# Kernel optimization log

Hardware: AMD Instinct MI355X
Metric: run time of the kernel (lower is better)

## Reference

```python
import jax, jax.numpy as jnp
import numpy as np

# Lorentz (hyperboloid) manifold, curvature parameter K: x0 = sqrt(K + ||x_space||^2)
K = 1.0
LN_EPS = 1e-5
PROJ_EPS = 1e-6
L, D, H, B, S, V = 12, 512, 8, 2, 1024, 50257
DH = D // H  # 64 space dims per head


def add_time(space):
    # lift space components onto the hyperboloid
    t = jnp.sqrt(jnp.sum(space * space, axis=-1, keepdims=True) + K)
    return jnp.concatenate([t, space], axis=-1)


def l_project(z):
    # renormalize an ambient vector onto the hyperboloid (Lorentz midpoint / LResNet normalization)
    inner = -jnp.square(z[..., :1]) + jnp.sum(jnp.square(z[..., 1:]), axis=-1, keepdims=True)
    return jnp.sqrt(K) * z / jnp.sqrt(jnp.clip(-inner, PROJ_EPS, None))


def l_layernorm(x, g, b):
    # LayerNorm on the space part, recompute time
    s = x[..., 1:]
    mu = jnp.mean(s, axis=-1, keepdims=True)
    var = jnp.var(s, axis=-1, keepdims=True)
    s = (s - mu) * jax.lax.rsqrt(var + LN_EPS) * g + b
    return add_time(s)


def setup_inputs() -> dict:
    key = jax.random.key(0)
    ks = jax.random.split(key, 12)
    std_in = D ** -0.5
    std_out = (2 * D * L) ** -0.5  # out_proj_std from the torch init
    inp = {}
    inp['text_tokens'] = jax.random.randint(ks[0], (B, S), 0, V)
    inp['embed_table'] = jax.random.normal(ks[1], (V, D - 1), jnp.float32) * 0.02
    inp['Wq'] = jax.random.normal(ks[2], (L, D, D), jnp.float32) * std_in
    inp['bq'] = jnp.zeros((L, D), jnp.float32)
    inp['Wk'] = jax.random.normal(ks[3], (L, D, D), jnp.float32) * std_in
    inp['bk'] = jnp.zeros((L, D), jnp.float32)
    inp['Wv'] = jax.random.normal(ks[4], (L, D, D), jnp.float32) * std_in
    inp['bv'] = jnp.zeros((L, D), jnp.float32)
    inp['Wo'] = jax.random.normal(ks[5], (L, H * (DH + 1), D - 1), jnp.float32) * std_in
    inp['bo'] = jnp.zeros((L, D - 1), jnp.float32)
    inp['ln1_g'] = jnp.ones((L, D - 1), jnp.float32)
    inp['ln1_b'] = jnp.zeros((L, D - 1), jnp.float32)
    inp['ln2_g'] = jnp.ones((L, D - 1), jnp.float32)
    inp['ln2_b'] = jnp.zeros((L, D - 1), jnp.float32)
    inp['Wfc'] = jax.random.normal(ks[6], (L, D, 4 * D - 1), jnp.float32) * std_in
    inp['bfc'] = jnp.zeros((L, 4 * D - 1), jnp.float32)
    inp['Wpr'] = jax.random.normal(ks[7], (L, 4 * D, D - 1), jnp.float32) * std_out
    inp['bpr'] = jnp.zeros((L, D - 1), jnp.float32)
    inp['res_w1'] = jnp.ones((L,), jnp.float32)
    inp['res_w2'] = jnp.ones((L,), jnp.float32)
    inp['Wfin'] = jax.random.normal(ks[8], (D, D - 1), jnp.float32) * std_in
    inp['bfin'] = jnp.zeros((D - 1,), jnp.float32)
    inp['lnf_g'] = jnp.ones((D - 1,), jnp.float32)
    inp['lnf_b'] = jnp.zeros((D - 1,), jnp.float32)
    return inp


def reference(text_tokens, embed_table, Wq, bq, Wk, bk, Wv, bv, Wo, bo, ln1_g, ln1_b,
              ln2_g, ln2_b, Wfc, bfc, Wpr, bpr, res_w1, res_w2, Wfin, bfin, lnf_g, lnf_b):
    b, s = text_tokens.shape
    scale = 1.0 / np.sqrt(DH)
    # LorentzEmbeddings: space-part lookup, time recomputed
    x = add_time(embed_table[text_tokens])  # [B, S, D]
    causal = jnp.tril(jnp.ones((s, s), bool))  # True = attend
    for i in range(L):
        # --- Lorentz multi-head self-attention ---
        lx = l_layernorm(x, ln1_g[i], ln1_b[i])
        q = add_time((lx @ Wq[i] + bq[i]).reshape(b, s, H, DH))  # [B,S,H,DH+1]
        k = add_time((lx @ Wk[i] + bk[i]).reshape(b, s, H, DH))
        v = add_time((lx @ Wv[i] + bv[i]).reshape(b, s, H, DH))
        qm = jnp.concatenate([-q[..., :1], q[..., 1:]], axis=-1)  # apply Minkowski metric
        linner = jnp.einsum('bihd,bjhd->bhij', qm, k)  # Lorentz inner product <q_i, k_j>_L
        scores = (2.0 * K + 2.0 * linner) * scale     # = -d_L^2(q,k)/sqrt(dh)
        scores = jnp.where(causal[None, None], scores, -1e9)
        a = jax.nn.softmax(scores, axis=-1)
        agg = jnp.einsum('bhij,bjhd->bihd', a, v)      # Lorentz centroid numerator
        agg = l_project(agg)                           # normalize back to hyperboloid
        ax = add_time(agg.reshape(b, s, H * (DH + 1)) @ Wo[i] + bo[i])  # heads-concat proj
        x = l_project(x + res_w1[i] * ax)              # LResNet residual 1
        # --- Lorentz MLP ---
        h = l_layernorm(x, ln2_g[i], ln2_b[i])
        h = add_time(h @ Wfc[i] + bfc[i])              # c_fc: D -> 4D ambient
        h = add_time(jax.nn.gelu(h[..., 1:]))          # LorentzActivation (GELU on space)
        h = add_time(h @ Wpr[i] + bpr[i])              # c_proj: 4D -> D ambient
        x = l_project(x + res_w2[i] * h)               # LResNet residual 2
    x = add_time(x @ Wfin + bfin)                      # final_proj
    x = l_layernorm(x, lnf_g, lnf_b)                   # ln_final
    return x
```

## Files before the change

kernel.cpp:

```cpp
#include <hip/hip_runtime.h>
#include <cstdint>

#define DEV __device__ __forceinline__

typedef _Float16 f16;
typedef _Float16 f16x8 __attribute__((ext_vector_type(8)));
typedef float f32x4 __attribute__((ext_vector_type(4)));
typedef unsigned int u32;

DEV void gll16(const void* g, void* l) {
  __builtin_amdgcn_global_load_lds((const __attribute__((address_space(1))) u32*)g,
                                   (__attribute__((address_space(3))) u32*)l, 16, 0, 0);
}

DEV float block_sum(float v, float* red) {
#pragma unroll
  for (int o = 32; o; o >>= 1) v += __shfl_xor(v, o);
  int w = threadIdx.x >> 6;
  __syncthreads();
  if ((threadIdx.x & 63) == 0) red[w] = v;
  __syncthreads();
  return red[0] + red[1] + red[2] + red[3];
}

__global__ void k_trans(const float* __restrict__ W, f16* __restrict__ BT, int K, int N, int Kpad) {
  __shared__ float t[32][33];
  int n0 = blockIdx.x * 32, k0 = blockIdx.y * 32, tx = threadIdx.x, ty = threadIdx.y;
  for (int i = ty; i < 32; i += 8) {
    int k = k0 + i, n = n0 + tx;
    t[i][tx] = (k < K && n < N) ? W[(size_t)k * N + n] : 0.f;
  }
  __syncthreads();
  for (int i = ty; i < 32; i += 8)
    BT[(size_t)(n0 + i) * Kpad + k0 + tx] = (f16)t[tx][i];
}

__global__ void k_trans3(const float* __restrict__ Wq, const float* __restrict__ Wk,
                         const float* __restrict__ Wv, f16* __restrict__ BT) {
  __shared__ float t[32][33];
  const float* W = (blockIdx.z == 0) ? Wq : (blockIdx.z == 1) ? Wk : Wv;
  f16* dst = BT + (size_t)blockIdx.z * 512 * 512;
  int n0 = blockIdx.x * 32, k0 = blockIdx.y * 32, tx = threadIdx.x, ty = threadIdx.y;
  for (int i = ty; i < 32; i += 8) t[i][tx] = W[(size_t)(k0 + i) * 512 + n0 + tx];
  __syncthreads();
  for (int i = ty; i < 32; i += 8) dst[(size_t)(n0 + i) * 512 + k0 + tx] = (f16)t[tx][i];
}

template <int BM, int BN>
__launch_bounds__(256)
__global__ void k_gemm(const f16* __restrict__ A, const f16* __restrict__ BT,
                       float* __restrict__ C, int K, int Nstride) {
  constexpr int BK = 32;
  constexpr int FM = BM / 32, FN = BN / 32;
  __shared__ f16 sA[BM * BK];
  __shared__ f16 sB[BN * BK];
  const int tid = threadIdx.x, wid = tid >> 6, lane = tid & 63;
  const int m0 = blockIdx.x * BM, n0 = blockIdx.y * BN;
  const int wm = wid >> 1, wn = wid & 1;
  f32x4 acc[FM][FN];
#pragma unroll
  for (int i = 0; i < FM; i++)
#pragma unroll
    for (int j = 0; j < FN; j++) acc[i][j] = (f32x4){0.f, 0.f, 0.f, 0.f};
  const char* Ab = (const char*)A + (size_t)m0 * K * 2;
  const char* Bb = (const char*)BT + (size_t)n0 * K * 2;
  const size_t rowB = (size_t)K * 2;
  for (int k0 = 0; k0 < K; k0 += BK) {
    for (int i = wid; i < BM / 16; i += 4)
      gll16(Ab + (size_t)(i * 16 + (lane >> 2)) * rowB + k0 * 2 + (lane & 3) * 16,
            (char*)sA + i * 1024);
    for (int i = wid; i < BN / 16; i += 4)
      gll16(Bb + (size_t)(i * 16 + (lane >> 2)) * rowB + k0 * 2 + (lane & 3) * 16,
            (char*)sB + i * 1024);
    __syncthreads();
    f16x8 af[FM], bfr[FN];
#pragma unroll
    for (int i = 0; i < FM; i++)
      af[i] = *(const f16x8*)(sA + (wm * (BM / 2) + i * 16 + (lane & 15)) * BK + (lane >> 4) * 8);
#pragma unroll
    for (int j = 0; j < FN; j++)
      bfr[j] = *(const f16x8*)(sB + (wn * (BN / 2) + j * 16 + (lane & 15)) * BK + (lane >> 4) * 8);
#pragma unroll
    for (int i = 0; i < FM; i++)
#pragma unroll
      for (int j = 0; j < FN; j++)
        acc[i][j] = __builtin_amdgcn_mfma_f32_16x16x32_f16(af[i], bfr[j], acc[i][j], 0, 0, 0);
    __syncthreads();
  }
#pragma unroll
  for (int i = 0; i < FM; i++) {
    int row0 = m0 + wm * (BM / 2) + i * 16 + ((lane >> 4) * 4);
#pragma unroll
    for (int j = 0; j < FN; j++) {
      int col = n0 + wn * (BN / 2) + j * 16 + (lane & 15);
#pragma unroll
      for (int r = 0; r < 4; r++) C[(size_t)(row0 + r) * Nstride + col] = acc[i][j][r];
    }
  }
}

__global__ void k_embed(const int* __restrict__ tok, const float* __restrict__ tbl,
                        const float* __restrict__ g, const float* __restrict__ bsh,
                        float* __restrict__ x, f16* __restrict__ act) {
  __shared__ float red[4];
  const int m = blockIdx.x, tid = threadIdx.x;
  const float* e = tbl + (size_t)tok[m] * 511;
  float e0 = (tid < 511) ? e[tid] : 0.f;
  float e1 = (tid + 256 < 511) ? e[tid + 256] : 0.f;
  float s1 = block_sum(e0 + e1, red);
  float s2 = block_sum(e0 * e0 + e1 * e1, red);
  float t = sqrtf(s2 + 1.f);
  float* xr = x + (size_t)m * 512;
  if (tid == 0) xr[0] = t;
  if (tid < 511) xr[1 + tid] = e0;
  if (tid + 256 < 511) xr[257 + tid] = e1;
  float mu = s1 / 511.f;
  float var = s2 / 511.f - mu * mu;
  float inv = rsqrtf(var + 1e-5f);
  float n0 = (tid < 511) ? (e0 - mu) * inv * g[tid] + bsh[tid] : 0.f;
  float n1 = (tid + 256 < 511) ? (e1 - mu) * inv * g[tid + 256] + bsh[tid + 256] : 0.f;
  float sn = block_sum(n0 * n0 + n1 * n1, red);
  float t2 = sqrtf(sn + 1.f);
  f16* ar = act + (size_t)m * 512;
  if (tid == 0) ar[0] = (f16)t2;
  if (tid < 511) ar[1 + tid] = (f16)n0;
  if (tid + 256 < 511) ar[257 + tid] = (f16)n1;
}

__launch_bounds__(64)
__global__ void k_qkvsplit(const float* __restrict__ raw, const float* __restrict__ bq,
                           const float* __restrict__ bk, const float* __restrict__ bv,
                           f16* __restrict__ qhat, f16* __restrict__ khat, f16* __restrict__ vT) {
  const int m = blockIdx.x, grp = blockIdx.y, typ = grp >> 3, h = grp & 7, lane = threadIdx.x;
  const float* bb = (typ == 0) ? bq : (typ == 1) ? bk : bv;
  float v = raw[(size_t)m * 1536 + typ * 512 + h * 64 + lane] + bb[h * 64 + lane];
  float s2 = v * v;
#pragma unroll
  for (int o = 32; o; o >>= 1) s2 += __shfl_xor(s2, o);
  float t = sqrtf(s2 + 1.0f);
  const int b = m >> 10, s = m & 1023, bh = b * 8 + h;
  if (typ == 0) {
    size_t base = ((size_t)bh * 1024 + s) * 88;
    qhat[base + lane] = (f16)(0.25f * v);
    if (lane == 0) qhat[base + 64] = (f16)(0.25f * t);
  } else if (typ == 1) {
    size_t base = ((size_t)bh * 1024 + s) * 88;
    khat[base + lane] = (f16)v;
    if (lane == 0) khat[base + 64] = (f16)t;
  } else {
    vT[((size_t)bh * 80 + lane) * 1024 + s] = (f16)v;
    if (lane == 0) vT[((size_t)bh * 80 + 64) * 1024 + s] = (f16)t;
  }
}

__launch_bounds__(256)
__global__ void k_attn(const f16* __restrict__ qhat, const f16* __restrict__ khat,
                       const f16* __restrict__ vT, f16* __restrict__ ao) {
  __shared__ f16 sK[64 * 88];
  __shared__ f16 sV[80 * 72];
  __shared__ f16 sP[4][16 * 80];
  const int bh = blockIdx.x, qt = blockIdx.y, q0 = qt * 64;
  const int tid = threadIdx.x, wid = tid >> 6, lane = tid & 63;
  const int l15 = lane & 15, l4 = lane >> 4;
  const f16* qpl = qhat + (size_t)bh * 1024 * 88;
  const f16* kpl = khat + (size_t)bh * 1024 * 88;
  const f16* vpl = vT + (size_t)bh * 80 * 1024;
  const int qrow = q0 + wid * 16;
  f16x8 qf0 = *(const f16x8*)(qpl + (size_t)(qrow + l15) * 88 + l4 * 8);
  f16x8 qf1 = *(const f16x8*)(qpl + (size_t)(qrow + l15) * 88 + 32 + l4 * 8);
  float qth[4];
#pragma unroll
  for (int r = 0; r < 4; r++) qth[r] = (float)qpl[(size_t)(qrow + l4 * 4 + r) * 88 + 64];
  f32x4 acc[5];
#pragma unroll
  for (int i = 0; i < 5; i++) acc[i] = (f32x4){0, 0, 0, 0};
  float mrun[4] = {-3e38f, -3e38f, -3e38f, -3e38f}, lrun[4] = {0, 0, 0, 0};
  const int ntiles = qt + 1;
  for (int jt = 0; jt < ntiles; ++jt) {
    int j0 = jt * 64;
    for (int i = wid; i < 11; i += 4)
      gll16((const char*)kpl + (size_t)j0 * 176 + i * 1024 + lane * 16, (char*)sK + i * 1024);
    for (int idx = tid; idx < 640; idx += 256) {
      int row = idx >> 3, c = idx & 7;
      *(int4*)(sV + row * 72 + c * 8) = *(const int4*)(vpl + (size_t)row * 1024 + j0 + c * 8);
    }
    __syncthreads();
    f32x4 sc[4];
#pragma unroll
    for (int fn = 0; fn < 4; fn++) {
      const f16* kb = sK + (fn * 16 + l15) * 88;
      f16x8 k0v = *(const f16x8*)(kb + l4 * 8);
      f16x8 k1v = *(const f16x8*)(kb + 32 + l4 * 8);
      f32x4 a = (f32x4){0, 0, 0, 0};
      a = __builtin_amdgcn_mfma_f32_16x16x32_f16(qf0, k0v, a, 0, 0, 0);
      a = __builtin_amdgcn_mfma_f32_16x16x32_f16(qf1, k1v, a, 0, 0, 0);
      sc[fn] = a;
    }
    float s[4][4];
#pragma unroll
    for (int fn = 0; fn < 4; fn++) {
      float ktc = (float)sK[(fn * 16 + l15) * 88 + 64];
      int col = j0 + fn * 16 + l15;
#pragma unroll
      for (int r = 0; r < 4; r++) {
        int row = q0 + wid * 16 + l4 * 4 + r;
        float v = sc[fn][r] - qth[r] * ktc;
        s[fn][r] = (col <= row) ? v : -3e38f;
      }
    }
    float mnew[4], al[4], rs[4];
#pragma unroll
    for (int r = 0; r < 4; r++) {
      float t = fmaxf(fmaxf(s[0][r], s[1][r]), fmaxf(s[2][r], s[3][r]));
#pragma unroll
      for (int o = 8; o; o >>= 1) t = fmaxf(t, __shfl_xor(t, o));
      mnew[r] = fmaxf(mrun[r], t);
      al[r] = exp2f((mrun[r] - mnew[r]) * 1.44269504f);
      mrun[r] = mnew[r];
      rs[r] = 0.f;
    }
    f16* sPw = sP[wid];
#pragma unroll
    for (int fn = 0; fn < 4; fn++)
#pragma unroll
      for (int r = 0; r < 4; r++) {
        float p = exp2f((s[fn][r] - mnew[r]) * 1.44269504f);
        rs[r] += p;
        sPw[(l4 * 4 + r) * 80 + fn * 16 + l15] = (f16)p;
      }
#pragma unroll
    for (int r = 0; r < 4; r++) {
#pragma unroll
      for (int o = 8; o; o >>= 1) rs[r] += __shfl_xor(rs[r], o);
      lrun[r] = lrun[r] * al[r] + rs[r];
    }
#pragma unroll
    for (int fd = 0; fd < 5; fd++)
#pragma unroll
      for (int r = 0; r < 4; r++) acc[fd][r] *= al[r];
#pragma unroll
    for (int ks = 0; ks < 2; ks++) {
      f16x8 pf = *(const f16x8*)(sPw + l15 * 80 + ks * 32 + l4 * 8);
#pragma unroll
      for (int fd = 0; fd < 5; fd++) {
        f16x8 vf = *(const f16x8*)(sV + (fd * 16 + l15) * 72 + ks * 32 + l4 * 8);
        acc[fd] = __builtin_amdgcn_mfma_f32_16x16x32_f16(pf, vf, acc[fd], 0, 0, 0);
      }
    }
    __syncthreads();
  }
  const int b = bh >> 3, h = bh & 7;
#pragma unroll
  for (int r = 0; r < 4; r++) {
    float invl = 1.0f / lrun[r];
    float ss = 0.f;
    float ov[4];
#pragma unroll
    for (int fd = 0; fd < 4; fd++) {
      ov[fd] = acc[fd][r] * invl;
      ss += ov[fd] * ov[fd];
    }
#pragma unroll
    for (int o = 8; o; o >>= 1) ss += __shfl_xor(ss, o);
    float tv = acc[4][r] * invl;
    tv = __shfl(tv, lane & 48);
    float scp = rsqrtf(fmaxf(tv * tv - ss, 1e-6f));
    int row = q0 + wid * 16 + l4 * 4 + r;
    size_t rb = ((size_t)b * 1024 + row) * 544 + h * 65;
    if (l15 == 0) ao[rb] = (f16)(tv * scp);
#pragma unroll
    for (int fd = 0; fd < 4; fd++) ao[rb + 1 + fd * 16 + l15] = (f16)(ov[fd] * scp);
  }
}

__global__ void k_resproj(float* __restrict__ x, const float* __restrict__ raw,
                          const float* __restrict__ bias, const float* __restrict__ resw, int li,
                          const float* __restrict__ g, const float* __restrict__ bsh,
                          f16* __restrict__ act, int applyLN) {
  __shared__ float red[4];
  const int m = blockIdx.x, tid = threadIdx.x;
  const float* rr = raw + (size_t)m * 512;
  float* xr = x + (size_t)m * 512;
  const float rw = resw[li];
  float y0 = (tid < 511) ? rr[tid] + bias[tid] : 0.f;
  float y1 = (tid + 256 < 511) ? rr[tid + 256] + bias[tid + 256] : 0.f;
  float s2 = block_sum(y0 * y0 + y1 * y1, red);
  float tax = sqrtf(s2 + 1.f);
  float xt = xr[0];
  float u0 = (tid < 511) ? xr[1 + tid] + rw * y0 : 0.f;
  float u1 = (tid + 256 < 511) ? xr[257 + tid] + rw * y1 : 0.f;
  float ut = xt + rw * tax;
  float su = block_sum(u0 + u1, red);
  float su2 = block_sum(u0 * u0 + u1 * u1, red);
  float scp = rsqrtf(fmaxf(ut * ut - su2, 1e-6f));
  float nx0 = u0 * scp, nx1 = u1 * scp, nxt = ut * scp;
  if (tid == 0) xr[0] = nxt;
  if (tid < 511) xr[1 + tid] = nx0;
  if (tid + 256 < 511) xr[257 + tid] = nx1;
  f16* ar = act + (size_t)m * 512;
  if (applyLN) {
    float mu = su * scp / 511.f;
    float var = su2 * scp * scp / 511.f - mu * mu;
    float inv = rsqrtf(var + 1e-5f);
    float n0 = (tid < 511) ? (nx0 - mu) * inv * g[tid] + bsh[tid] : 0.f;
    float n1 = (tid + 256 < 511) ? (nx1 - mu) * inv * g[tid + 256] + bsh[tid + 256] : 0.f;
    float sn = block_sum(n0 * n0 + n1 * n1, red);
    float t2 = sqrtf(sn + 1.f);
    if (tid == 0) ar[0] = (f16)t2;
    if (tid < 511) ar[1 + tid] = (f16)n0;
    if (tid + 256 < 511) ar[257 + tid] = (f16)n1;
  } else {
    if (tid == 0) ar[0] = (f16)nxt;
    if (tid < 511) ar[1 + tid] = (f16)nx0;
    if (tid + 256 < 511) ar[257 + tid] = (f16)nx1;
  }
}

__global__ void k_gelu(const float* __restrict__ raw, const float* __restrict__ bias,
                       f16* __restrict__ act) {
  __shared__ float red[4];
  const int m = blockIdx.x, tid = threadIdx.x;
  const float* rr = raw + (size_t)m * 2048;
  float gv[8];
  float s2 = 0.f;
#pragma unroll
  for (int i = 0; i < 8; i++) {
    int j = i * 256 + tid;
    float y = (j < 2047) ? rr[j] + bias[j] : 0.f;
    float c = y * y * y;
    float gg = 0.5f * y * (1.f + tanhf(0.7978845608f * (y + 0.044715f * c)));
    if (j >= 2047) gg = 0.f;
    gv[i] = gg;
    s2 += gg * gg;
  }
  s2 = block_sum(s2, red);
  float t = sqrtf(s2 + 1.f);
  f16* ar = act + (size_t)m * 2048;
  if (tid == 0) ar[0] = (f16)t;
#pragma unroll
  for (int i = 0; i < 8; i++) {
    int j = i * 256 + tid;
    if (j < 2047) ar[1 + j] = (f16)gv[i];
  }
}

__global__ void k_final(const float* __restrict__ raw, const float* __restrict__ bias,
                        const float* __restrict__ g, const float* __restrict__ bsh,
                        float* __restrict__ out) {
  __shared__ float red[4];
  const int m = blockIdx.x, tid = threadIdx.x;
  const float* rr = raw + (size_t)m * 512;
  float y0 = (tid < 511) ? rr[tid] + bias[tid] : 0.f;
  float y1 = (tid + 256 < 511) ? rr[tid + 256] + bias[tid + 256] : 0.f;
  float s1 = block_sum(y0 + y1, red);
  float s2 = block_sum(y0 * y0 + y1 * y1, red);
  float mu = s1 / 511.f;
  float var = s2 / 511.f - mu * mu;
  float inv = rsqrtf(var + 1e-5f);
  float n0 = (tid < 511) ? (y0 - mu) * inv * g[tid] + bsh[tid] : 0.f;
  float n1 = (tid + 256 < 511) ? (y1 - mu) * inv * g[tid + 256] + bsh[tid + 256] : 0.f;
  float sn = block_sum(n0 * n0 + n1 * n1, red);
  float t2 = sqrtf(sn + 1.f);
  float* orow = out + (size_t)m * 512;
  if (tid == 0) orow[0] = t2;
  if (tid < 511) orow[1 + tid] = n0;
  if (tid + 256 < 511) orow[257 + tid] = n1;
}

extern "C" void kernel_launch(void* const* d_in, const int* in_sizes, int n_in,
                              void* d_out, int out_size, void* d_ws, size_t ws_size,
                              hipStream_t stream) {
  (void)in_sizes; (void)n_in; (void)out_size; (void)ws_size;
  const int* tok = (const int*)d_in[0];
  const float* etab = (const float*)d_in[1];
  const float* Wq = (const float*)d_in[2];
  const float* bq = (const float*)d_in[3];
  const float* Wk = (const float*)d_in[4];
  const float* bk = (const float*)d_in[5];
  const float* Wv = (const float*)d_in[6];
  const float* bv = (const float*)d_in[7];
  const float* Wo = (const float*)d_in[8];
  const float* bo = (const float*)d_in[9];
  const float* ln1g = (const float*)d_in[10];
  const float* ln1b = (const float*)d_in[11];
  const float* ln2g = (const float*)d_in[12];
  const float* ln2b = (const float*)d_in[13];
  const float* Wfc = (const float*)d_in[14];
  const float* bfc = (const float*)d_in[15];
  const float* Wpr = (const float*)d_in[16];
  const float* bpr = (const float*)d_in[17];
  const float* rw1 = (const float*)d_in[18];
  const float* rw2 = (const float*)d_in[19];
  const float* Wfin = (const float*)d_in[20];
  const float* bfin = (const float*)d_in[21];
  const float* lnfg = (const float*)d_in[22];
  const float* lnfb = (const float*)d_in[23];

  char* wsb = (char*)d_ws;
  size_t off = 0;
  auto alloc = [&](size_t bytes) -> char* {
    char* p = wsb + off;
    off = (off + bytes + 1023) & ~(size_t)1023;
    return p;
  };
  float* x = (float*)alloc(2048ull * 512 * 4);
  f16* actA = (f16*)alloc(2048ull * 512 * 2);
  float* raw = (float*)alloc(2048ull * 2048 * 4);
  f16* qhat = (f16*)alloc(16ull * 1024 * 88 * 2);
  f16* khat = (f16*)alloc(16ull * 1024 * 88 * 2);
  f16* vT = (f16*)alloc(16ull * 80 * 1024 * 2);
  f16* ao = (f16*)alloc(2048ull * 544 * 2);
  f16* fcact = (f16*)alloc(2048ull * 2048 * 2);
  f16* wqkvT = (f16*)alloc(1536ull * 512 * 2);
  f16* woT = (f16*)alloc(512ull * 544 * 2);
  f16* wfcT = (f16*)alloc(2048ull * 512 * 2);
  f16* wprT = (f16*)alloc(512ull * 2048 * 2);
  f16* wfinT = (f16*)alloc(512ull * 512 * 2);

  k_embed<<<2048, 256, 0, stream>>>(tok, etab, ln1g, ln1b, x, actA);

  for (int li = 0; li < 12; li++) {
    const float* Wq_l = Wq + (size_t)li * 512 * 512;
    const float* Wk_l = Wk + (size_t)li * 512 * 512;
    const float* Wv_l = Wv + (size_t)li * 512 * 512;
    const float* Wo_l = Wo + (size_t)li * 520 * 511;
    const float* Wfc_l = Wfc + (size_t)li * 512 * 2047;
    const float* Wpr_l = Wpr + (size_t)li * 2048 * 511;
    const float* bq_l = bq + (size_t)li * 512;
    const float* bk_l = bk + (size_t)li * 512;
    const float* bv_l = bv + (size_t)li * 512;
    const float* bo_l = bo + (size_t)li * 511;
    const float* bfc_l = bfc + (size_t)li * 2047;
    const float* bpr_l = bpr + (size_t)li * 511;
    const float* ln2g_l = ln2g + (size_t)li * 511;
    const float* ln2b_l = ln2b + (size_t)li * 511;

    k_trans3<<<dim3(16, 16, 3), dim3(32, 8), 0, stream>>>(Wq_l, Wk_l, Wv_l, wqkvT);
    k_trans<<<dim3(16, 17), dim3(32, 8), 0, stream>>>(Wo_l, woT, 520, 511, 544);
    k_trans<<<dim3(64, 16), dim3(32, 8), 0, stream>>>(Wfc_l, wfcT, 512, 2047, 512);
    k_trans<<<dim3(16, 64), dim3(32, 8), 0, stream>>>(Wpr_l, wprT, 2048, 511, 2048);

    k_gemm<128, 128><<<dim3(16, 12), 256, 0, stream>>>(actA, wqkvT, raw, 512, 1536);
    k_qkvsplit<<<dim3(2048, 24), 64, 0, stream>>>(raw, bq_l, bk_l, bv_l, qhat, khat, vT);
    k_attn<<<dim3(16, 16), 256, 0, stream>>>(qhat, khat, vT, ao);
    k_gemm<64, 64><<<dim3(32, 8), 256, 0, stream>>>(ao, woT, raw, 544, 512);
    k_resproj<<<2048, 256, 0, stream>>>(x, raw, bo_l, rw1, li, ln2g_l, ln2b_l, actA, 1);
    k_gemm<128, 128><<<dim3(16, 16), 256, 0, stream>>>(actA, wfcT, raw, 512, 2048);
    k_gelu<<<2048, 256, 0, stream>>>(raw, bfc_l, fcact);
    k_gemm<64, 64><<<dim3(32, 8), 256, 0, stream>>>(fcact, wprT, raw, 2048, 512);
    const float* ng = (li < 11) ? ln1g + (size_t)(li + 1) * 511 : ln1g;
    const float* nb = (li < 11) ? ln1b + (size_t)(li + 1) * 511 : ln1b;
    k_resproj<<<2048, 256, 0, stream>>>(x, raw, bpr_l, rw2, li, ng, nb, actA, (li < 11) ? 1 : 0);
  }

  k_trans<<<dim3(16, 16), dim3(32, 8), 0, stream>>>(Wfin, wfinT, 512, 511, 512);
  k_gemm<64, 64><<<dim3(32, 8), 256, 0, stream>>>(actA, wfinT, raw, 512, 512);
  k_final<<<2048, 256, 0, stream>>>(raw, bfin, lnfg, lnfb, (float*)d_out);
}
```

Baseline: 1.953 ms.

## Fuse QKV split and GELU into GEMM epilogues, batch weight transposes, rework attention

```diff
diff --git a/kernel.cpp b/kernel.cpp
--- a/kernel.cpp
+++ b/kernel.cpp
@@ -23,8 +23,11 @@
   return red[0] + red[1] + red[2] + red[3];
 }
 
-__global__ void k_trans(const float* __restrict__ W, f16* __restrict__ BT, int K, int N, int Kpad) {
+__global__ void k_trans(const float* __restrict__ W0, f16* __restrict__ BT0, int K, int N, int Kpad,
+                        size_t srcStride, size_t dstStride) {
   __shared__ float t[32][33];
+  const float* W = W0 + (size_t)blockIdx.z * srcStride;
+  f16* BT = BT0 + (size_t)blockIdx.z * dstStride;
   int n0 = blockIdx.x * 32, k0 = blockIdx.y * 32, tx = threadIdx.x, ty = threadIdx.y;
   for (int i = ty; i < 32; i += 8) {
     int k = k0 + i, n = n0 + tx;
@@ -38,63 +41,157 @@
 __global__ void k_trans3(const float* __restrict__ Wq, const float* __restrict__ Wk,
                          const float* __restrict__ Wv, f16* __restrict__ BT) {
   __shared__ float t[32][33];
-  const float* W = (blockIdx.z == 0) ? Wq : (blockIdx.z == 1) ? Wk : Wv;
-  f16* dst = BT + (size_t)blockIdx.z * 512 * 512;
+  const int layer = blockIdx.z / 3, typ = blockIdx.z % 3;
+  const float* W = ((typ == 0) ? Wq : (typ == 1) ? Wk : Wv) + (size_t)layer * 262144;
+  f16* dst = BT + (size_t)layer * 786432 + (size_t)typ * 262144;
   int n0 = blockIdx.x * 32, k0 = blockIdx.y * 32, tx = threadIdx.x, ty = threadIdx.y;
   for (int i = ty; i < 32; i += 8) t[i][tx] = W[(size_t)(k0 + i) * 512 + n0 + tx];
   __syncthreads();
   for (int i = ty; i < 32; i += 8) dst[(size_t)(n0 + i) * 512 + k0 + tx] = (f16)t[tx][i];
 }
 
-template <int BM, int BN>
+template <int BM, int BN, int EPI>
 __launch_bounds__(256)
 __global__ void k_gemm(const f16* __restrict__ A, const f16* __restrict__ BT,
-                       float* __restrict__ C, int K, int Nstride) {
-  constexpr int BK = 32;
+                       int lda, int ldb, int klen,
+                       float* __restrict__ O1, float* __restrict__ O2, int ldc,
+                       const float* __restrict__ c0, const float* __restrict__ c1,
+                       const float* __restrict__ c2, float* __restrict__ ssq,
+                       f16* __restrict__ H1, f16* __restrict__ H2, f16* __restrict__ H3) {
   constexpr int FM = BM / 32, FN = BN / 32;
-  __shared__ f16 sA[BM * BK];
-  __shared__ f16 sB[BN * BK];
+  __shared__ f16 sA[BM * 64];
+  __shared__ f16 sB[BN * 64];
   const int tid = threadIdx.x, wid = tid >> 6, lane = tid & 63;
+  const int l15 = lane & 15, l4 = lane >> 4;
   const int m0 = blockIdx.x * BM, n0 = blockIdx.y * BN;
   const int wm = wid >> 1, wn = wid & 1;
+  const int kbeg = blockIdx.z * klen;
   f32x4 acc[FM][FN];
 #pragma unroll
   for (int i = 0; i < FM; i++)
 #pragma unroll
     for (int j = 0; j < FN; j++) acc[i][j] = (f32x4){0.f, 0.f, 0.f, 0.f};
-  const char* Ab = (const char*)A + (size_t)m0 * K * 2;
-  const char* Bb = (const char*)BT + (size_t)n0 * K * 2;
-  const size_t rowB = (size_t)K * 2;
-  for (int k0 = 0; k0 < K; k0 += BK) {
-    for (int i = wid; i < BM / 16; i += 4)
-      gll16(Ab + (size_t)(i * 16 + (lane >> 2)) * rowB + k0 * 2 + (lane & 3) * 16,
-            (char*)sA + i * 1024);
-    for (int i = wid; i < BN / 16; i += 4)
-      gll16(Bb + (size_t)(i * 16 + (lane >> 2)) * rowB + k0 * 2 + (lane & 3) * 16,
-            (char*)sB + i * 1024);
+  const size_t ldab = (size_t)lda * 2, ldbb = (size_t)ldb * 2;
+  const int swz = ((lane & 7) ^ (lane >> 3)) * 16;
+  const char* Ab = (const char*)A + (size_t)m0 * ldab + (size_t)(lane >> 3) * ldab + swz;
+  const char* Bb = (const char*)BT + (size_t)n0 * ldbb + (size_t)(lane >> 3) * ldbb + swz;
+  for (int k0 = kbeg; k0 < kbeg + klen; k0 += 64) {
+    for (int i = wid; i < BM / 8; i += 4)
+      gll16(Ab + (size_t)(i * 8) * ldab + (size_t)k0 * 2, (char*)sA + i * 1024);
+    for (int i = wid; i < BN / 8; i += 4)
+      gll16(Bb + (size_t)(i * 8) * ldbb + (size_t)k0 * 2, (char*)sB + i * 1024);
     __syncthreads();
-    f16x8 af[FM], bfr[FN];
-#pragma unroll
-    for (int i = 0; i < FM; i++)
-      af[i] = *(const f16x8*)(sA + (wm * (BM / 2) + i * 16 + (lane & 15)) * BK + (lane >> 4) * 8);
-#pragma unroll
-    for (int j = 0; j < FN; j++)
-      bfr[j] = *(const f16x8*)(sB + (wn * (BN / 2) + j * 16 + (lane & 15)) * BK + (lane >> 4) * 8);
-#pragma unroll
-    for (int i = 0; i < FM; i++)
-#pragma unroll
-      for (int j = 0; j < FN; j++)
-        acc[i][j] = __builtin_amdgcn_mfma_f32_16x16x32_f16(af[i], bfr[j], acc[i][j], 0, 0, 0);
+#pragma unroll
+    for (int kk = 0; kk < 2; kk++) {
+      f16x8 af[FM], bf[FN];
+#pragma unroll
+      for (int i = 0; i < FM; i++) {
+        int row = wm * (BM / 2) + i * 16 + l15;
+        af[i] = *(const f16x8*)(sA + row * 64 + (((kk * 4 + l4) ^ (l15 & 7)) * 8));
+      }
+#pragma unroll
+      for (int j = 0; j < FN; j++) {
+        int row = wn * (BN / 2) + j * 16 + l15;
+        bf[j] = *(const f16x8*)(sB + row * 64 + (((kk * 4 + l4) ^ (l15 & 7)) * 8));
+      }
+#pragma unroll
+      for (int i = 0; i < FM; i++)
+#pragma unroll
+        for (int j = 0; j < FN; j++)
+          acc[i][j] = __builtin_amdgcn_mfma_f32_16x16x32_f16(af[i], bf[j], acc[i][j], 0, 0, 0);
+    }
     __syncthreads();
   }
-#pragma unroll
-  for (int i = 0; i < FM; i++) {
-    int row0 = m0 + wm * (BM / 2) + i * 16 + ((lane >> 4) * 4);
-#pragma unroll
-    for (int j = 0; j < FN; j++) {
-      int col = n0 + wn * (BN / 2) + j * 16 + (lane & 15);
-#pragma unroll
-      for (int r = 0; r < 4; r++) C[(size_t)(row0 + r) * Nstride + col] = acc[i][j][r];
+  if (EPI == 0) {
+#pragma unroll
+    for (int i = 0; i < FM; i++) {
+      int row0 = m0 + wm * (BM / 2) + i * 16 + l4 * 4;
+#pragma unroll
+      for (int j = 0; j < FN; j++) {
+        int col = n0 + wn * (BN / 2) + j * 16 + l15;
+#pragma unroll
+        for (int r = 0; r < 4; r++) O1[(size_t)(row0 + r) * ldc + col] = acc[i][j][r];
+      }
+    }
+  } else if (EPI == 1) {
+    const int cb = (n0 >> 6) + wn;
+    const int typ = cb >> 3, h = cb & 7;
+    const float* bb = (typ == 0) ? c0 : (typ == 1) ? c1 : c2;
+    float bias_j[FN];
+#pragma unroll
+    for (int j = 0; j < FN; j++) bias_j[j] = bb[h * 64 + j * 16 + l15];
+    const float qs = (typ == 0) ? 0.25f : 1.0f;
+#pragma unroll
+    for (int i = 0; i < FM; i++) {
+#pragma unroll
+      for (int r = 0; r < 4; r++) {
+        float y[FN];
+        float ss = 0.f;
+#pragma unroll
+        for (int j = 0; j < FN; j++) {
+          y[j] = acc[i][j][r] + bias_j[j];
+          ss += y[j] * y[j];
+        }
+        ss += __shfl_xor(ss, 1); ss += __shfl_xor(ss, 2);
+        ss += __shfl_xor(ss, 4); ss += __shfl_xor(ss, 8);
+        float t = sqrtf(ss + 1.f);
+        int row = m0 + wm * 64 + i * 16 + l4 * 4 + r;
+        int b = row >> 10, s = row & 1023, bh = b * 8 + h;
+        if (typ < 2) {
+          f16* dst = (typ == 0) ? H1 : H2;
+          size_t base = ((size_t)bh * 1024 + s) * 88;
+#pragma unroll
+          for (int j = 0; j < FN; j++) dst[base + j * 16 + l15] = (f16)(qs * y[j]);
+          if (l15 == 0) dst[base + 64] = (f16)(qs * t);
+        } else {
+#pragma unroll
+          for (int j = 0; j < FN; j++)
+            H3[((size_t)bh * 80 + j * 16 + l15) * 1024 + s] = (f16)y[j];
+          if (l15 == 0) H3[((size_t)bh * 80 + 64) * 1024 + s] = (f16)t;
+        }
+      }
+    }
+  } else if (EPI == 2) {
+#pragma unroll
+    for (int i = 0; i < FM; i++) {
+#pragma unroll
+      for (int r = 0; r < 4; r++) {
+        int row = m0 + wm * 64 + i * 16 + l4 * 4 + r;
+        float ss = 0.f;
+#pragma unroll
+        for (int j = 0; j < FN; j++) {
+          int col = n0 + wn * 64 + j * 16 + l15;
+          float gg = 0.f;
+          if (col < 2047) {
+            float yv = acc[i][j][r] + c0[col];
+            float cc = yv * yv * yv;
+            gg = 0.5f * yv * (1.f + tanhf(0.7978845608f * (yv + 0.044715f * cc)));
+          }
+          ss += gg * gg;
+          H1[(size_t)row * 2048 + col] = (f16)gg;
+        }
+        ss += __shfl_xor(ss, 1); ss += __shfl_xor(ss, 2);
+        ss += __shfl_xor(ss, 4); ss += __shfl_xor(ss, 8);
+        if (l15 == 0) atomicAdd(ssq + row, ss);
+      }
+    }
+  } else {
+    float* O = blockIdx.z ? O2 : O1;
+#pragma unroll
+    for (int i = 0; i < FM; i++) {
+#pragma unroll
+      for (int r = 0; r < 4; r++) {
+        int row = m0 + wm * (BM / 2) + i * 16 + l4 * 4 + r;
+        float t = 0.f;
+        if (blockIdx.z == 0) t = sqrtf(ssq[row] + 1.f);
+#pragma unroll
+        for (int j = 0; j < FN; j++) {
+          int col = n0 + wn * (BN / 2) + j * 16 + l15;
+          float v = acc[i][j][r];
+          if (blockIdx.z == 0) v += t * ((col < 511) ? c0[col] : 0.f);
+          O[(size_t)row * ldc + col] = v;
+        }
+      }
     }
   }
 }
@@ -128,67 +225,31 @@
 }
 
 __launch_bounds__(64)
-__global__ void k_qkvsplit(const float* __restrict__ raw, const float* __restrict__ bq,
-                           const float* __restrict__ bk, const float* __restrict__ bv,
-                           f16* __restrict__ qhat, f16* __restrict__ khat, f16* __restrict__ vT) {
-  const int m = blockIdx.x, grp = blockIdx.y, typ = grp >> 3, h = grp & 7, lane = threadIdx.x;
-  const float* bb = (typ == 0) ? bq : (typ == 1) ? bk : bv;
-  float v = raw[(size_t)m * 1536 + typ * 512 + h * 64 + lane] + bb[h * 64 + lane];
-  float s2 = v * v;
-#pragma unroll
-  for (int o = 32; o; o >>= 1) s2 += __shfl_xor(s2, o);
-  float t = sqrtf(s2 + 1.0f);
-  const int b = m >> 10, s = m & 1023, bh = b * 8 + h;
-  if (typ == 0) {
-    size_t base = ((size_t)bh * 1024 + s) * 88;
-    qhat[base + lane] = (f16)(0.25f * v);
-    if (lane == 0) qhat[base + 64] = (f16)(0.25f * t);
-  } else if (typ == 1) {
-    size_t base = ((size_t)bh * 1024 + s) * 88;
-    khat[base + lane] = (f16)v;
-    if (lane == 0) khat[base + 64] = (f16)t;
-  } else {
-    vT[((size_t)bh * 80 + lane) * 1024 + s] = (f16)v;
-    if (lane == 0) vT[((size_t)bh * 80 + 64) * 1024 + s] = (f16)t;
-  }
-}
-
-__launch_bounds__(256)
 __global__ void k_attn(const f16* __restrict__ qhat, const f16* __restrict__ khat,
                        const f16* __restrict__ vT, f16* __restrict__ ao) {
-  __shared__ f16 sK[64 * 88];
-  __shared__ f16 sV[80 * 72];
-  __shared__ f16 sP[4][16 * 80];
-  const int bh = blockIdx.x, qt = blockIdx.y, q0 = qt * 64;
-  const int tid = threadIdx.x, wid = tid >> 6, lane = tid & 63;
-  const int l15 = lane & 15, l4 = lane >> 4;
-  const f16* qpl = qhat + (size_t)bh * 1024 * 88;
-  const f16* kpl = khat + (size_t)bh * 1024 * 88;
-  const f16* vpl = vT + (size_t)bh * 80 * 1024;
-  const int qrow = q0 + wid * 16;
-  f16x8 qf0 = *(const f16x8*)(qpl + (size_t)(qrow + l15) * 88 + l4 * 8);
-  f16x8 qf1 = *(const f16x8*)(qpl + (size_t)(qrow + l15) * 88 + 32 + l4 * 8);
+  __shared__ f16 sP[16 * 88];
+  const int bid = blockIdx.x, bh = bid & 15, rt = 63 - (bid >> 4);
+  const int lane = threadIdx.x, l15 = lane & 15, l4 = lane >> 4;
+  const f16* qp = qhat + ((size_t)bh * 1024 + rt * 16) * 88;
+  const f16* kp = khat + (size_t)bh * 1024 * 88;
+  const f16* vp = vT + (size_t)bh * 80 * 1024;
+  f16x8 qf0 = *(const f16x8*)(qp + l15 * 88 + l4 * 8);
+  f16x8 qf1 = *(const f16x8*)(qp + l15 * 88 + 32 + l4 * 8);
   float qth[4];
 #pragma unroll
-  for (int r = 0; r < 4; r++) qth[r] = (float)qpl[(size_t)(qrow + l4 * 4 + r) * 88 + 64];
+  for (int r = 0; r < 4; r++) qth[r] = (float)qp[(l4 * 4 + r) * 88 + 64];
   f32x4 acc[5];
 #pragma unroll
   for (int i = 0; i < 5; i++) acc[i] = (f32x4){0, 0, 0, 0};
   float mrun[4] = {-3e38f, -3e38f, -3e38f, -3e38f}, lrun[4] = {0, 0, 0, 0};
-  const int ntiles = qt + 1;
-  for (int jt = 0; jt < ntiles; ++jt) {
-    int j0 = jt * 64;
-    for (int i = wid; i < 11; i += 4)
-      gll16((const char*)kpl + (size_t)j0 * 176 + i * 1024 + lane * 16, (char*)sK + i * 1024);
-    for (int idx = tid; idx < 640; idx += 256) {
-      int row = idx >> 3, c = idx & 7;
-      *(int4*)(sV + row * 72 + c * 8) = *(const int4*)(vpl + (size_t)row * 1024 + j0 + c * 8);
-    }
-    __syncthreads();
+  const int nt = (rt >> 2) + 1;
+  for (int jt = 0; jt < nt; ++jt) {
+    const int j0 = jt * 64;
+    const bool dt = (jt == nt - 1);
     f32x4 sc[4];
 #pragma unroll
     for (int fn = 0; fn < 4; fn++) {
-      const f16* kb = sK + (fn * 16 + l15) * 88;
+      const f16* kb = kp + (size_t)(j0 + fn * 16 + l15) * 88;
       f16x8 k0v = *(const f16x8*)(kb + l4 * 8);
       f16x8 k1v = *(const f16x8*)(kb + 32 + l4 * 8);
       f32x4 a = (f32x4){0, 0, 0, 0};
@@ -199,13 +260,13 @@
     float s[4][4];
 #pragma unroll
     for (int fn = 0; fn < 4; fn++) {
-      float ktc = (float)sK[(fn * 16 + l15) * 88 + 64];
+      float ktc = (float)kp[(size_t)(j0 + fn * 16 + l15) * 88 + 64];
       int col = j0 + fn * 16 + l15;
 #pragma unroll
       for (int r = 0; r < 4; r++) {
-        int row = q0 + wid * 16 + l4 * 4 + r;
+        int row = rt * 16 + l4 * 4 + r;
         float v = sc[fn][r] - qth[r] * ktc;
-        s[fn][r] = (col <= row) ? v : -3e38f;
+        s[fn][r] = (!dt || col <= row) ? v : -3e38f;
       }
     }
     float mnew[4], al[4], rs[4];
@@ -219,14 +280,13 @@
       mrun[r] = mnew[r];
       rs[r] = 0.f;
     }
-    f16* sPw = sP[wid];
 #pragma unroll
     for (int fn = 0; fn < 4; fn++)
 #pragma unroll
       for (int r = 0; r < 4; r++) {
         float p = exp2f((s[fn][r] - mnew[r]) * 1.44269504f);
         rs[r] += p;
-        sPw[(l4 * 4 + r) * 80 + fn * 16 + l15] = (f16)p;
+        sP[(l4 * 4 + r) * 88 + fn * 16 + l15] = (f16)p;
       }
 #pragma unroll
     for (int r = 0; r < 4; r++) {
@@ -238,12 +298,13 @@
     for (int fd = 0; fd < 5; fd++)
 #pragma unroll
       for (int r = 0; r < 4; r++) acc[fd][r] *= al[r];
+    __syncthreads();
 #pragma unroll
     for (int ks = 0; ks < 2; ks++) {
-      f16x8 pf = *(const f16x8*)(sPw + l15 * 80 + ks * 32 + l4 * 8);
+      f16x8 pf = *(const f16x8*)(sP + l15 * 88 + ks * 32 + l4 * 8);
 #pragma unroll
       for (int fd = 0; fd < 5; fd++) {
-        f16x8 vf = *(const f16x8*)(sV + (fd * 16 + l15) * 72 + ks * 32 + l4 * 8);
+        f16x8 vf = *(const f16x8*)(vp + (size_t)(fd * 16 + l15) * 1024 + j0 + ks * 32 + l4 * 8);
         acc[fd] = __builtin_amdgcn_mfma_f32_16x16x32_f16(pf, vf, acc[fd], 0, 0, 0);
       }
     }
@@ -265,25 +326,31 @@
     float tv = acc[4][r] * invl;
     tv = __shfl(tv, lane & 48);
     float scp = rsqrtf(fmaxf(tv * tv - ss, 1e-6f));
-    int row = q0 + wid * 16 + l4 * 4 + r;
-    size_t rb = ((size_t)b * 1024 + row) * 544 + h * 65;
+    int row = rt * 16 + l4 * 4 + r;
+    size_t rowbase = ((size_t)b * 1024 + row) * 576;
+    size_t rb = rowbase + h * 65;
     if (l15 == 0) ao[rb] = (f16)(tv * scp);
 #pragma unroll
     for (int fd = 0; fd < 4; fd++) ao[rb + 1 + fd * 16 + l15] = (f16)(ov[fd] * scp);
-  }
-}
-
-__global__ void k_resproj(float* __restrict__ x, const float* __restrict__ raw,
+    for (int c = l15; c < 56; c += 16) ao[rowbase + 520 + c] = (f16)0.f;
+  }
+}
+
+__global__ void k_resproj(float* __restrict__ x, const float* __restrict__ r1,
+                          const float* __restrict__ r2, int useR2,
                           const float* __restrict__ bias, const float* __restrict__ resw, int li,
                           const float* __restrict__ g, const float* __restrict__ bsh,
-                          f16* __restrict__ act, int applyLN) {
+                          f16* __restrict__ act, int applyLN, float* __restrict__ ssq) {
   __shared__ float red[4];
   const int m = blockIdx.x, tid = threadIdx.x;
-  const float* rr = raw + (size_t)m * 512;
+  const float* ra = r1 + (size_t)m * 512;
+  const float* rb = r2 + (size_t)m * 512;
   float* xr = x + (size_t)m * 512;
   const float rw = resw[li];
-  float y0 = (tid < 511) ? rr[tid] + bias[tid] : 0.f;
-  float y1 = (tid + 256 < 511) ? rr[tid + 256] + bias[tid + 256] : 0.f;
+  if (tid == 0) ssq[m] = 0.f;
+  float y0 = 0.f, y1 = 0.f;
+  if (tid < 511) { y0 = ra[tid] + bias[tid]; if (useR2) y0 += rb[tid]; }
+  if (tid + 256 < 511) { y1 = ra[tid + 256] + bias[tid + 256]; if (useR2) y1 += rb[tid + 256]; }
   float s2 = block_sum(y0 * y0 + y1 * y1, red);
   float tax = sqrtf(s2 + 1.f);
   float xt = xr[0];
@@ -316,34 +383,6 @@
   }
 }
 
-__global__ void k_gelu(const float* __restrict__ raw, const float* __restrict__ bias,
-                       f16* __restrict__ act) {
-  __shared__ float red[4];
-  const int m = blockIdx.x, tid = threadIdx.x;
-  const float* rr = raw + (size_t)m * 2048;
-  float gv[8];
-  float s2 = 0.f;
-#pragma unroll
-  for (int i = 0; i < 8; i++) {
-    int j = i * 256 + tid;
-    float y = (j < 2047) ? rr[j] + bias[j] : 0.f;
-    float c = y * y * y;
-    float gg = 0.5f * y * (1.f + tanhf(0.7978845608f * (y + 0.044715f * c)));
-    if (j >= 2047) gg = 0.f;
-    gv[i] = gg;
-    s2 += gg * gg;
-  }
-  s2 = block_sum(s2, red);
-  float t = sqrtf(s2 + 1.f);
-  f16* ar = act + (size_t)m * 2048;
-  if (tid == 0) ar[0] = (f16)t;
-#pragma unroll
-  for (int i = 0; i < 8; i++) {
-    int j = i * 256 + tid;
-    if (j < 2047) ar[1 + j] = (f16)gv[i];
-  }
-}
-
 __global__ void k_final(const float* __restrict__ raw, const float* __restrict__ bias,
                         const float* __restrict__ g, const float* __restrict__ bsh,
                         float* __restrict__ out) {
@@ -405,26 +444,36 @@
   };
   float* x = (float*)alloc(2048ull * 512 * 4);
   f16* actA = (f16*)alloc(2048ull * 512 * 2);
-  float* raw = (float*)alloc(2048ull * 2048 * 4);
+  float* raw1 = (float*)alloc(2048ull * 512 * 4);
+  float* raw2 = (float*)alloc(2048ull * 512 * 4);
+  float* ssq = (float*)alloc(2048ull * 4);
   f16* qhat = (f16*)alloc(16ull * 1024 * 88 * 2);
   f16* khat = (f16*)alloc(16ull * 1024 * 88 * 2);
   f16* vT = (f16*)alloc(16ull * 80 * 1024 * 2);
-  f16* ao = (f16*)alloc(2048ull * 544 * 2);
+  f16* ao = (f16*)alloc(2048ull * 576 * 2);
   f16* fcact = (f16*)alloc(2048ull * 2048 * 2);
-  f16* wqkvT = (f16*)alloc(1536ull * 512 * 2);
-  f16* woT = (f16*)alloc(512ull * 544 * 2);
-  f16* wfcT = (f16*)alloc(2048ull * 512 * 2);
-  f16* wprT = (f16*)alloc(512ull * 2048 * 2);
+  f16* wqkvT = (f16*)alloc(12ull * 1536 * 512 * 2);
+  f16* woT = (f16*)alloc(12ull * 512 * 576 * 2);
+  f16* wfcT = (f16*)alloc(12ull * 2048 * 512 * 2);
+  f16* wprT = (f16*)alloc(12ull * 512 * 2048 * 2);
   f16* wfinT = (f16*)alloc(512ull * 512 * 2);
 
+  k_trans3<<<dim3(16, 16, 36), dim3(32, 8), 0, stream>>>(Wq, Wk, Wv, wqkvT);
+  k_trans<<<dim3(16, 18, 12), dim3(32, 8), 0, stream>>>(Wo, woT, 520, 511, 576,
+                                                        520ull * 511, 512ull * 576);
+  k_trans<<<dim3(64, 16, 12), dim3(32, 8), 0, stream>>>(Wfc, wfcT, 512, 2047, 512,
+                                                        512ull * 2047, 2048ull * 512);
+  k_trans<<<dim3(16, 64, 12), dim3(32, 8), 0, stream>>>(Wpr + 511, wprT, 2047, 511, 2048,
+                                                        2048ull * 511, 512ull * 2048);
+  k_trans<<<dim3(16, 16, 1), dim3(32, 8), 0, stream>>>(Wfin, wfinT, 512, 511, 512, 0, 0);
+
   k_embed<<<2048, 256, 0, stream>>>(tok, etab, ln1g, ln1b, x, actA);
 
   for (int li = 0; li < 12; li++) {
-    const float* Wq_l = Wq + (size_t)li * 512 * 512;
-    const float* Wk_l = Wk + (size_t)li * 512 * 512;
-    const float* Wv_l = Wv + (size_t)li * 512 * 512;
-    const float* Wo_l = Wo + (size_t)li * 520 * 511;
-    const float* Wfc_l = Wfc + (size_t)li * 512 * 2047;
+    const f16* wqkvT_l = wqkvT + (size_t)li * 1536 * 512;
+    const f16* woT_l = woT + (size_t)li * 512 * 576;
+    const f16* wfcT_l = wfcT + (size_t)li * 2048 * 512;
+    const f16* wprT_l = wprT + (size_t)li * 512 * 2048;
     const float* Wpr_l = Wpr + (size_t)li * 2048 * 511;
     const float* bq_l = bq + (size_t)li * 512;
     const float* bk_l = bk + (size_t)li * 512;
@@ -435,25 +484,29 @@
     const float* ln2g_l = ln2g + (size_t)li * 511;
     const float* ln2b_l = ln2b + (size_t)li * 511;
 
-    k_trans3<<<dim3(16, 16, 3), dim3(32, 8), 0, stream>>>(Wq_l, Wk_l, Wv_l, wqkvT);
-    k_trans<<<dim3(16, 17), dim3(32, 8), 0, stream>>>(Wo_l, woT, 520, 511, 544);
-    k_trans<<<dim3(64, 16), dim3(32, 8), 0, stream>>>(Wfc_l, wfcT, 512, 2047, 512);
-    k_trans<<<dim3(16, 64), dim3(32, 8), 0, stream>>>(Wpr_l, wprT, 2048, 511, 2048);
-
-    k_gemm<128, 128><<<dim3(16, 12), 256, 0, stream>>>(actA, wqkvT, raw, 512, 1536);
-    k_qkvsplit<<<dim3(2048, 24), 64, 0, stream>>>(raw, bq_l, bk_l, bv_l, qhat, khat, vT);
-    k_attn<<<dim3(16, 16), 256, 0, stream>>>(qhat, khat, vT, ao);
-    k_gemm<64, 64><<<dim3(32, 8), 256, 0, stream>>>(ao, woT, raw, 544, 512);
-    k_resproj<<<2048, 256, 0, stream>>>(x, raw, bo_l, rw1, li, ln2g_l, ln2b_l, actA, 1);
-    k_gemm<128, 128><<<dim3(16, 16), 256, 0, stream>>>(actA, wfcT, raw, 512, 2048);
-    k_gelu<<<2048, 256, 0, stream>>>(raw, bfc_l, fcact);
-    k_gemm<64, 64><<<dim3(32, 8), 256, 0, stream>>>(fcact, wprT, raw, 2048, 512);
+    k_gemm<128, 128, 1><<<dim3(16, 12, 1), 256, 0, stream>>>(
+        actA, wqkvT_l, 512, 512, 512, nullptr, nullptr, 0,
+        bq_l, bk_l, bv_l, nullptr, qhat, khat, vT);
+    k_attn<<<1024, 64, 0, stream>>>(qhat, khat, vT, ao);
+    k_gemm<64, 64, 0><<<dim3(32, 8, 1), 256, 0, stream>>>(
+        ao, woT_l, 576, 576, 576, raw1, nullptr, 512,
+        nullptr, nullptr, nullptr, nullptr, nullptr, nullptr, nullptr);
+    k_resproj<<<2048, 256, 0, stream>>>(x, raw1, raw1, 0, bo_l, rw1, li,
+                                        ln2g_l, ln2b_l, actA, 1, ssq);
+    k_gemm<128, 128, 2><<<dim3(16, 16, 1), 256, 0, stream>>>(
+        actA, wfcT_l, 512, 512, 512, nullptr, nullptr, 0,
+        bfc_l, nullptr, nullptr, ssq, fcact, nullptr, nullptr);
+    k_gemm<64, 64, 3><<<dim3(32, 8, 2), 256, 0, stream>>>(
+        fcact, wprT_l, 2048, 2048, 1024, raw1, raw2, 512,
+        Wpr_l, nullptr, nullptr, ssq, nullptr, nullptr, nullptr);
     const float* ng = (li < 11) ? ln1g + (size_t)(li + 1) * 511 : ln1g;
     const float* nb = (li < 11) ? ln1b + (size_t)(li + 1) * 511 : ln1b;
-    k_resproj<<<2048, 256, 0, stream>>>(x, raw, bpr_l, rw2, li, ng, nb, actA, (li < 11) ? 1 : 0);
-  }
-
-  k_trans<<<dim3(16, 16), dim3(32, 8), 0, stream>>>(Wfin, wfinT, 512, 511, 512);
-  k_gemm<64, 64><<<dim3(32, 8), 256, 0, stream>>>(actA, wfinT, raw, 512, 512);
-  k_final<<<2048, 256, 0, stream>>>(raw, bfin, lnfg, lnfb, (float*)d_out);
-}
+    k_resproj<<<2048, 256, 0, stream>>>(x, raw1, raw2, 1, bpr_l, rw2, li,
+                                        ng, nb, actA, (li < 11) ? 1 : 0, ssq);
+  }
+
+  k_gemm<64, 64, 0><<<dim3(32, 8, 1), 256, 0, stream>>>(
+      actA, wfinT, 512, 512, 512, raw1, nullptr, 512,
+      nullptr, nullptr, nullptr, nullptr, nullptr, nullptr, nullptr);
+  k_final<<<2048, 256, 0, stream>>>(raw1, bfin, lnfg, lnfb, (float*)d_out);
+}
```

New measurement: 1.650 ms. -15.5%, faster.
